# Performance work log

Measured on AMD Instinct MI355X. Metric: run time of the kernel, lower is better.

## Reference

```python
import jax, jax.numpy as jnp
import numpy as np

IN_CH = 512
HEADS = 8
DIM_HEAD = 64
HIDDEN = HEADS * DIM_HEAD


def rms_norm(x, g):
    # torch F.normalize(x, dim=1): x / max(||x||_2 along channel, eps)
    norm = jnp.sqrt(jnp.sum(x * x, axis=1, keepdims=True))
    xn = x / jnp.maximum(norm, 1e-12)
    return xn * g * (x.shape[1] ** 0.5)


def setup_inputs() -> dict:
    key = jax.random.key(0)
    ks = jax.random.split(key, 6)
    x = jax.random.normal(ks[0], (8, IN_CH, 8192), dtype=jnp.float32)
    g1 = jnp.ones((1, IN_CH, 1), dtype=jnp.float32)
    # Conv1d k=1 weights stored as [out, in]
    w_qkv = jax.random.normal(ks[1], (3 * HIDDEN, IN_CH), dtype=jnp.float32) * (IN_CH ** -0.5)
    w_out = jax.random.normal(ks[2], (IN_CH, HIDDEN), dtype=jnp.float32) * (HIDDEN ** -0.5)
    b_out = jax.random.normal(ks[3], (IN_CH,), dtype=jnp.float32) * 0.01
    g2 = jnp.ones((1, IN_CH, 1), dtype=jnp.float32)
    return {"x": x, "g1": g1, "w_qkv": w_qkv, "w_out": w_out, "b_out": b_out, "g2": g2}


def reference(x, g1, w_qkv, w_out, b_out, g2):
    b, c, l = x.shape
    h, dh = HEADS, DIM_HEAD
    scale = dh ** -0.5
    xn = rms_norm(x, g1)
    # 1x1 conv == channel matmul: [b,3*hidden,l]
    qkv = jnp.einsum('oc,bcl->bol', w_qkv, xn)
    q, k, v = jnp.split(qkv, 3, axis=1)
    q = q.reshape(b, h, dh, l)
    k = k.reshape(b, h, dh, l)
    v = v.reshape(b, h, dh, l)
    q = jax.nn.softmax(q, axis=2) * scale  # softmax over head-dim channels
    k = jax.nn.softmax(k, axis=3)          # softmax over sequence
    context = jnp.einsum('bhdn,bhen->bhde', k, v)  # [b,h,dh,dh]
    out = jnp.einsum('bhde,bhdn->bhen', context, q)
    out = out.reshape(b, h * dh, l)
    out = jnp.einsum('oc,bcl->bol', w_out, out) + b_out[None, :, None]
    return rms_norm(out, g2)
```

## Files before the change

kernel.cpp:

```cpp
#include <hip/hip_runtime.h>
#include <hip/hip_bf16.h>


typedef short short8 __attribute__((ext_vector_type(8)));
typedef short short4v __attribute__((ext_vector_type(4)));
typedef float f32x4 __attribute__((ext_vector_type(4)));
typedef unsigned short ushort;

#define SQRT512 22.627416997969522f

__device__ __forceinline__ ushort f2bf(float f){
  union{float f; unsigned u;} v; v.f = f;
  unsigned r = v.u + 0x7fffu + ((v.u >> 16) & 1u);
  return (ushort)(r >> 16);
}

__device__ __forceinline__ void gload16(const void* g, void* l){
  __builtin_amdgcn_global_load_lds(
      (const __attribute__((address_space(1))) unsigned int*)(unsigned long long)g,
      (__attribute__((address_space(3))) unsigned int*)(unsigned int)(unsigned long long)l,
      16, 0, 0);
}

__global__ void k_prep_w1(const float* __restrict__ wqkv, const float* __restrict__ g1,
                          ushort* __restrict__ W1){
  int i = blockIdx.x * 256 + threadIdx.x;
  int c = i & 511;
  W1[i] = f2bf(wqkv[i] * g1[c] * SQRT512);
}

__global__ __launch_bounds__(256) void k_xt(const float* __restrict__ x,
                                            ushort* __restrict__ Xt,
                                            float* __restrict__ invnorm){
  __shared__ __align__(16) ushort tile[64*132];
  __shared__ float ssq[4][64];
  int b = blockIdx.y, lb = blockIdx.x;
  int t = threadIdx.x, lane = t & 63, crow = t >> 6;
  const float* xb = x + ((size_t)b*512)*8192 + (size_t)lb*64;
  float acc = 0.f;
  for(int c0 = 0; c0 < 512; c0 += 128){
    __syncthreads();
    for(int cc = crow; cc < 128; cc += 4){
      float v = xb[(size_t)(c0+cc)*8192 + lane];
      acc += v*v;
      tile[lane*132 + cc] = f2bf(v);
    }
    __syncthreads();
    ushort* dst = Xt + ((size_t)(b*8192 + lb*64))*512 + c0;
    int ch = t & 31;
    for(int r = t >> 5; r < 64; r += 8){
      short4v vv = *(const short4v*)&tile[r*132 + ch*4];
      *(short4v*)(dst + (size_t)r*512 + ch*4) = vv;
    }
  }
  ssq[crow][lane] = acc;
  __syncthreads();
  if(t < 64){
    float s = ssq[0][t] + ssq[1][t] + ssq[2][t] + ssq[3][t];
    invnorm[b*8192 + lb*64 + t] = 1.f / fmaxf(sqrtf(s), 1e-12f);
  }
}

__global__ __launch_bounds__(512,1) void k_qkv(
    const ushort* __restrict__ W1, const ushort* __restrict__ Xt,
    const float* __restrict__ invnorm,
    ushort* __restrict__ Qt, float* __restrict__ ctxp, float* __restrict__ kpart){
  __shared__ __align__(16) union U {
    ushort buf[2][24576];
    struct { ushort P[16384]; ushort Vb[16384]; } e;
  } S;
  __shared__ float ksum[128];

  int bid = blockIdx.x;
  int wg  = (bid & 7)*384 + (bid >> 3);
  int b   = wg / 384;
  int rem = wg % 384;
  bool isQ = rem < 128;
  int t = threadIdx.x, lane = t & 63, w = t >> 6;
  int rsub = lane >> 3;
  int pc   = (lane & 7) ^ rsub;

  int r = 0, ct2 = 0, hb = 0, ct = 0;
  const ushort* Abase = W1;
  const ushort* Bbase;
  if(isQ){ r = rem >> 5; ct2 = rem & 31;
    Abase = W1 + (size_t)(r*128)*512;
    Bbase = Xt + ((size_t)(b*8192 + ct2*256))*512;
  } else { int kv = rem - 128; hb = kv >> 6; ct = kv & 63;
    Bbase = Xt + ((size_t)(b*8192 + ct*128))*512;
  }
  if(t < 128) ksum[t] = 0.f;

  f32x4 acc[4][4] = {};

  auto stage = [&](int ks, int cb){
    int goff = ks*64 + pc*8;
    ushort* A  = S.buf[cb];
    ushort* Bl = S.buf[cb] + (isQ ? 8192 : 16384);
    if(isQ){
#pragma unroll
      for(int j = 0; j < 2; ++j){ int m = w*2 + j;
        gload16(Abase + (size_t)(m*8 + rsub)*512 + goff, A + m*512); }
#pragma unroll
      for(int j = 0; j < 4; ++j){ int m = w*4 + j;
        gload16(Bbase + (size_t)(m*8 + rsub)*512 + goff, Bl + m*512); }
    } else {
#pragma unroll
      for(int j = 0; j < 4; ++j){ int m = w*4 + j;
        int row = (m < 16) ? (512 + hb*128 + m*8 + rsub)
                           : (1024 + hb*128 + (m-16)*8 + rsub);
        gload16(W1 + (size_t)row*512 + goff, A + m*512); }
#pragma unroll
      for(int j = 0; j < 2; ++j){ int m = w*2 + j;
        gload16(Bbase + (size_t)(m*8 + rsub)*512 + goff, Bl + m*512); }
    }
  };

  auto compute = [&](int cb){
    ushort* A  = S.buf[cb];
    ushort* Bl = S.buf[cb] + (isQ ? 8192 : 16384);
    int aw = isQ ? (w >> 2) : (w >> 1);
    int bw = isQ ? (w & 3)  : (w & 1);
#pragma unroll
    for(int kk = 0; kk < 2; ++kk){
      int g = kk*4 + (lane >> 4);
      short8 af[4], bf[4];
#pragma unroll
      for(int m4 = 0; m4 < 4; ++m4){ int ra = aw*64 + m4*16 + (lane & 15);
        af[m4] = *(const short8*)&A[ra*64 + (g ^ (ra & 7))*8]; }
#pragma unroll
      for(int n4 = 0; n4 < 4; ++n4){ int rb = bw*64 + n4*16 + (lane & 15);
        bf[n4] = *(const short8*)&Bl[rb*64 + (g ^ (rb & 7))*8]; }
#pragma unroll
      for(int m4 = 0; m4 < 4; ++m4)
#pragma unroll
        for(int n4 = 0; n4 < 4; ++n4)
          acc[m4][n4] = __builtin_amdgcn_mfma_f32_16x16x32_bf16(af[m4], bf[n4], acc[m4][n4], 0,0,0);
    }
  };

  stage(0, 0);
  int cur = 0;
#pragma unroll
  for(int ks = 0; ks < 8; ++ks){
    if(ks < 7) stage(ks + 1, cur ^ 1);
    if(ks < 7) asm volatile("s_waitcnt vmcnt(6)" ::: "memory");
    else       asm volatile("s_waitcnt vmcnt(0)" ::: "memory");
    __builtin_amdgcn_s_barrier();
    compute(cur);
    asm volatile("s_waitcnt lgkmcnt(0)" ::: "memory");
    __builtin_amdgcn_s_barrier();
    cur ^= 1;
  }

  if(isQ){
    int wr = w >> 2, wc = w & 3;
    float cs[4];
    const float* invb = invnorm + b*8192 + ct2*256;
#pragma unroll
    for(int n4 = 0; n4 < 4; ++n4) cs[n4] = invb[wc*64 + n4*16 + (lane & 15)];
    float mx[4] = {-3e38f,-3e38f,-3e38f,-3e38f};
#pragma unroll
    for(int m4 = 0; m4 < 4; ++m4)
#pragma unroll
      for(int n4 = 0; n4 < 4; ++n4)
#pragma unroll
        for(int j = 0; j < 4; ++j){
          float v = acc[m4][n4][j]*cs[n4];
          acc[m4][n4][j] = v;
          mx[n4] = fmaxf(mx[n4], v);
        }
#pragma unroll
    for(int n4 = 0; n4 < 4; ++n4){
      mx[n4] = fmaxf(mx[n4], __shfl_xor(mx[n4], 16));
      mx[n4] = fmaxf(mx[n4], __shfl_xor(mx[n4], 32));
    }
    float sm[4] = {0.f,0.f,0.f,0.f};
#pragma unroll
    for(int m4 = 0; m4 < 4; ++m4)
#pragma unroll
      for(int n4 = 0; n4 < 4; ++n4)
#pragma unroll
        for(int j = 0; j < 4; ++j){
          float e = __expf(acc[m4][n4][j] - mx[n4]);
          acc[m4][n4][j] = e;
          sm[n4] += e;
        }
    float inv[4];
#pragma unroll
    for(int n4 = 0; n4 < 4; ++n4){
      sm[n4] += __shfl_xor(sm[n4], 16);
      sm[n4] += __shfl_xor(sm[n4], 32);
      inv[n4] = 0.125f / sm[n4];
    }
#pragma unroll
    for(int n4 = 0; n4 < 4; ++n4){
      int col = ct2*256 + wc*64 + n4*16 + (lane & 15);
      ushort* dst = Qt + ((size_t)(b*8192 + col))*512 + r*128 + wr*64 + (lane >> 4)*4;
#pragma unroll
      for(int m4 = 0; m4 < 4; ++m4){
        short4v p;
#pragma unroll
        for(int j = 0; j < 4; ++j) p[j] = (short)f2bf(acc[m4][n4][j]*inv[n4]);
        *(short4v*)(dst + m4*16) = p;
      }
    }
  } else {
    int wr2 = w >> 1, bw = w & 1;
    bool isK = (w < 4);
    float cs[4];
    const float* invb = invnorm + b*8192 + ct*128;
#pragma unroll
    for(int n4 = 0; n4 < 4; ++n4) cs[n4] = invb[bw*64 + n4*16 + (lane & 15)];
#pragma unroll
    for(int m4 = 0; m4 < 4; ++m4)
#pragma unroll
      for(int j = 0; j < 4; ++j){
        int row = wr2*64 + m4*16 + (lane >> 4)*4 + j;
        float rs = 0.f;
#pragma unroll
        for(int n4 = 0; n4 < 4; ++n4){
          int lcol = bw*64 + n4*16 + (lane & 15);
          float val = acc[m4][n4][j]*cs[n4];
          if(isK){
            float e = __expf(val); rs += e;
            S.e.P[row*128 + ((lcol >> 3) ^ (row & 7))*8 + (lcol & 7)] = f2bf(e);
          } else {
            int er = row - 128;
            S.e.Vb[er*128 + ((lcol >> 3) ^ (er & 7))*8 + (lcol & 7)] = f2bf(val);
          }
        }
        if(isK) atomicAdd(&ksum[row], rs);
      }
    __syncthreads();
    if(t < 128) kpart[(size_t)ct*4096 + b*512 + hb*128 + t] = ksum[t];
    int hq = w >> 2, rq = w & 3;
    f32x4 c2[4] = {};
#pragma unroll
    for(int kk = 0; kk < 4; ++kk){
      int g = kk*4 + (lane >> 4);
      int da = hq*64 + rq*16 + (lane & 15);
      short8 pa = *(const short8*)&S.e.P[da*128 + (g ^ (da & 7))*8];
#pragma unroll
      for(int n4 = 0; n4 < 4; ++n4){
        int eb = hq*64 + n4*16 + (lane & 15);
        short8 vb = *(const short8*)&S.e.Vb[eb*128 + (g ^ (eb & 7))*8];
        c2[n4] = __builtin_amdgcn_mfma_f32_16x16x32_bf16(pa, vb, c2[n4], 0,0,0);
      }
    }
    float* dst = ctxp + ((size_t)((b*8 + hb*2 + hq)*64 + ct))*4096;
#pragma unroll
    for(int n4 = 0; n4 < 4; ++n4)
#pragma unroll
      for(int j = 0; j < 4; ++j){
        int d64 = rq*16 + (lane >> 4)*4 + j;
        int e   = n4*16 + (lane & 15);
        dst[d64*64 + e] = c2[n4][j];
      }
  }
}

__global__ void k_invz(const float* __restrict__ kpart, float* __restrict__ invZ){
  int row = blockIdx.x*256 + threadIdx.x;
  float s = 0.f;
  for(int c = 0; c < 64; ++c) s += kpart[(size_t)c*4096 + row];
  invZ[row] = 1.f / s;
}

__global__ void k_m2(const float* __restrict__ ctxp, const float* __restrict__ invZ,
                     const float* __restrict__ Wout, ushort* __restrict__ M2){
  __shared__ __align__(16) ushort ctxl[4096];
  int bh = blockIdx.x, b = bh >> 3, h = bh & 7;
  int t = threadIdx.x, lane = t & 63, w = t >> 6;
  for(int i = t; i < 4096; i += 512){
    float s = 0.f;
    for(int sp = 0; sp < 64; ++sp) s += ctxp[((size_t)(bh*64 + sp))*4096 + i];
    int d = i >> 6, e = i & 63;
    s *= invZ[bh*64 + d];
    ctxl[(e >> 3)*512 + d*8 + (e & 7)] = f2bf(s);
  }
  __syncthreads();
  f32x4 acc[4][4] = {};
#pragma unroll
  for(int kk = 0; kk < 2; ++kk){
    int g = kk*4 + (lane >> 4);
    short8 bf[4];
#pragma unroll
    for(int n4 = 0; n4 < 4; ++n4)
      bf[n4] = *(const short8*)&ctxl[g*512 + (n4*16 + (lane & 15))*8];
    int e0 = (lane >> 4)*8 + kk*32;
#pragma unroll
    for(int m4 = 0; m4 < 4; ++m4){
      int o = w*64 + m4*16 + (lane & 15);
      const float* wp = Wout + (size_t)o*512 + h*64 + e0;
      float4 w0 = *(const float4*)(wp);
      float4 w1 = *(const float4*)(wp + 4);
      short8 af;
      af[0]=(short)f2bf(w0.x); af[1]=(short)f2bf(w0.y); af[2]=(short)f2bf(w0.z); af[3]=(short)f2bf(w0.w);
      af[4]=(short)f2bf(w1.x); af[5]=(short)f2bf(w1.y); af[6]=(short)f2bf(w1.z); af[7]=(short)f2bf(w1.w);
#pragma unroll
      for(int n4 = 0; n4 < 4; ++n4)
        acc[m4][n4] = __builtin_amdgcn_mfma_f32_16x16x32_bf16(af, bf[n4], acc[m4][n4], 0,0,0);
    }
  }
  ushort* dst = M2 + (size_t)b*512*512 + h*64;
#pragma unroll
  for(int m4 = 0; m4 < 4; ++m4)
#pragma unroll
    for(int n4 = 0; n4 < 4; ++n4)
#pragma unroll
      for(int j = 0; j < 4; ++j){
        int o = w*64 + m4*16 + (lane >> 4)*4 + j;
        int d = n4*16 + (lane & 15);
        dst[(size_t)o*512 + d] = f2bf(acc[m4][n4][j]);
      }
}

__global__ __launch_bounds__(512,2) void k_out(const ushort* __restrict__ M2,
                                               const ushort* __restrict__ Qt,
                                               const float* __restrict__ bout,
                                               const float* __restrict__ g2,
                                               float* __restrict__ out){
  __shared__ __align__(16) ushort A[16384];
  __shared__ __align__(16) ushort Bs[2048];
  __shared__ float colss[64];
  __shared__ float bo[512], gg[512];
  int bid = blockIdx.x;
  int wg = (bid & 7)*128 + (bid >> 3);
  int b = wg >> 7, lb = wg & 127;
  int t = threadIdx.x, lane = t & 63, w = t >> 6;
  bo[t & 511] = bout[t & 511];
  gg[t & 511] = g2[t & 511];
  if(t < 64) colss[t] = 0.f;
  const ushort* Abase = M2 + (size_t)b*262144;
  const ushort* Bbase = Qt + ((size_t)(b*8192 + lb*64))*512;
  int rsub = lane >> 2;
  int pc   = (lane & 3) ^ ((lane >> 3) & 3);
  f32x4 acc[4][4] = {};
  for(int ks = 0; ks < 16; ++ks){
    int goff = ks*32 + pc*8;
#pragma unroll
    for(int j = 0; j < 4; ++j){
      int m = w*4 + j;
      gload16(Abase + (size_t)(m*16 + rsub)*512 + goff, &A[m*512]);
    }
    if(w >= 4){
      int m = w - 4;
      gload16(Bbase + (size_t)(m*16 + rsub)*512 + goff, &Bs[m*512]);
    }
    __syncthreads();
    int g = lane >> 4;
    short8 bf[4];
#pragma unroll
    for(int n4 = 0; n4 < 4; ++n4){
      int rb = n4*16 + (lane & 15);
      bf[n4] = *(const short8*)&Bs[rb*32 + (g ^ ((rb >> 1) & 3))*8];
    }
#pragma unroll
    for(int m4 = 0; m4 < 4; ++m4){
      int ra = w*64 + m4*16 + (lane & 15);
      short8 af = *(const short8*)&A[ra*32 + (g ^ ((ra >> 1) & 3))*8];
#pragma unroll
      for(int n4 = 0; n4 < 4; ++n4)
        acc[m4][n4] = __builtin_amdgcn_mfma_f32_16x16x32_bf16(af, bf[n4], acc[m4][n4], 0,0,0);
    }
    __syncthreads();
  }
  float ps[4] = {0.f,0.f,0.f,0.f};
#pragma unroll
  for(int m4 = 0; m4 < 4; ++m4)
#pragma unroll
    for(int j = 0; j < 4; ++j){
      int o = w*64 + m4*16 + (lane >> 4)*4 + j;
      float bb = bo[o];
#pragma unroll
      for(int n4 = 0; n4 < 4; ++n4){
        float v = acc[m4][n4][j] + bb;
        acc[m4][n4][j] = v;
        ps[n4] += v*v;
      }
    }
#pragma unroll
  for(int n4 = 0; n4 < 4; ++n4) atomicAdd(&colss[n4*16 + (lane & 15)], ps[n4]);
  __syncthreads();
  float csc[4];
#pragma unroll
  for(int n4 = 0; n4 < 4; ++n4)
    csc[n4] = SQRT512 / fmaxf(sqrtf(colss[n4*16 + (lane & 15)]), 1e-12f);
  float* obase = out + ((size_t)b*512)*8192 + lb*64;
#pragma unroll
  for(int m4 = 0; m4 < 4; ++m4)
#pragma unroll
    for(int j = 0; j < 4; ++j){
      int o = w*64 + m4*16 + (lane >> 4)*4 + j;
      float gv = gg[o];
#pragma unroll
      for(int n4 = 0; n4 < 4; ++n4)
        obase[(size_t)o*8192 + n4*16 + (lane & 15)] = acc[m4][n4][j]*csc[n4]*gv;
    }
}

extern "C" void kernel_launch(void* const* d_in, const int* in_sizes, int n_in,
                              void* d_out, int out_size, void* d_ws, size_t ws_size,
                              hipStream_t stream){
  const float* x    = (const float*)d_in[0];
  const float* g1   = (const float*)d_in[1];
  const float* wqkv = (const float*)d_in[2];
  const float* wout = (const float*)d_in[3];
  const float* bout = (const float*)d_in[4];
  const float* g2   = (const float*)d_in[5];
  float* out = (float*)d_out;
  char* ws = (char*)d_ws;
  const size_t MB = 1024*1024;
  ushort* Qt      = (ushort*)(ws);
  float*  ctxp    = (float*) (ws + 64*MB);
  ushort* W1      = (ushort*)(ws + 132*MB);
  float*  invnorm = (float*) (ws + 134*MB);
  float*  kpart   = (float*) (ws + 135*MB);
  float*  invZ    = (float*) (ws + 136*MB);
  ushort* M2      = (ushort*)(ws + 137*MB);
  ushort* Xt = (ushort*)d_out;

  k_prep_w1<<<3072, 256, 0, stream>>>(wqkv, g1, W1);
  k_xt<<<dim3(128, 8), 256, 0, stream>>>(x, Xt, invnorm);
  k_qkv<<<3072, 512, 0, stream>>>(W1, Xt, invnorm, Qt, ctxp, kpart);
  k_invz<<<16, 256, 0, stream>>>(kpart, invZ);
  k_m2<<<64, 512, 0, stream>>>(ctxp, invZ, wout, M2);
  k_out<<<1024, 512, 0, stream>>>(M2, Qt, bout, g2, out);
}
```

Measured before the change: 402.7 us.

## Halve k_qkv LDS footprint to allow more resident blocks per CU

```diff
diff --git a/kernel.cpp b/kernel.cpp
--- a/kernel.cpp
+++ b/kernel.cpp
@@ -61,13 +61,13 @@
   }
 }
 
-__global__ __launch_bounds__(512,1) void k_qkv(
+__global__ __launch_bounds__(512,4) void k_qkv(
     const ushort* __restrict__ W1, const ushort* __restrict__ Xt,
     const float* __restrict__ invnorm,
     ushort* __restrict__ Qt, float* __restrict__ ctxp, float* __restrict__ kpart){
   __shared__ __align__(16) union U {
-    ushort buf[2][24576];
-    struct { ushort P[16384]; ushort Vb[16384]; } e;
+    ushort buf[2][12288];
+    struct { ushort P[8192]; ushort Vb[8192]; } e;
   } S;
   __shared__ float ksum[128];
 
@@ -75,18 +75,19 @@
   int wg  = (bid & 7)*384 + (bid >> 3);
   int b   = wg / 384;
   int rem = wg % 384;
-  bool isQ = rem < 128;
+  int grp = rem / 12, s = rem % 12;
+  bool isQ = (s < 4);
   int t = threadIdx.x, lane = t & 63, w = t >> 6;
-  int rsub = lane >> 3;
-  int pc   = (lane & 7) ^ rsub;
+  int rsub = lane >> 2;
+  int pc   = (lane & 3) ^ ((lane >> 3) & 3);
 
   int r = 0, ct2 = 0, hb = 0, ct = 0;
-  const ushort* Abase = W1;
+  const ushort* Aq = W1;
   const ushort* Bbase;
-  if(isQ){ r = rem >> 5; ct2 = rem & 31;
-    Abase = W1 + (size_t)(r*128)*512;
+  if(isQ){ r = s; ct2 = grp;
+    Aq = W1 + (size_t)(r*128)*512;
     Bbase = Xt + ((size_t)(b*8192 + ct2*256))*512;
-  } else { int kv = rem - 128; hb = kv >> 6; ct = kv & 63;
+  } else { int t2 = s - 4; ct = 2*grp + (t2 & 1); hb = t2 >> 1;
     Bbase = Xt + ((size_t)(b*8192 + ct*128))*512;
   }
   if(t < 128) ksum[t] = 0.f;
@@ -94,63 +95,54 @@
   f32x4 acc[4][4] = {};
 
   auto stage = [&](int ks, int cb){
-    int goff = ks*64 + pc*8;
-    ushort* A  = S.buf[cb];
-    ushort* Bl = S.buf[cb] + (isQ ? 8192 : 16384);
+    int goff = ks*32 + pc*8;
     if(isQ){
-#pragma unroll
-      for(int j = 0; j < 2; ++j){ int m = w*2 + j;
-        gload16(Abase + (size_t)(m*8 + rsub)*512 + goff, A + m*512); }
-#pragma unroll
-      for(int j = 0; j < 4; ++j){ int m = w*4 + j;
-        gload16(Bbase + (size_t)(m*8 + rsub)*512 + goff, Bl + m*512); }
+      ushort* A  = S.buf[cb];
+      ushort* Bl = S.buf[cb] + 4096;
+      gload16(Aq    + (size_t)(w*16 + rsub)*512 + goff, A + w*512);
+      gload16(Bbase + (size_t)(w*32 + rsub)*512 + goff, Bl + w*1024);
+      gload16(Bbase + (size_t)(w*32 + 16 + rsub)*512 + goff, Bl + w*1024 + 512);
     } else {
-#pragma unroll
-      for(int j = 0; j < 4; ++j){ int m = w*4 + j;
-        int row = (m < 16) ? (512 + hb*128 + m*8 + rsub)
-                           : (1024 + hb*128 + (m-16)*8 + rsub);
-        gload16(W1 + (size_t)row*512 + goff, A + m*512); }
-#pragma unroll
-      for(int j = 0; j < 2; ++j){ int m = w*2 + j;
-        gload16(Bbase + (size_t)(m*8 + rsub)*512 + goff, Bl + m*512); }
+      ushort* A  = S.buf[cb];
+      ushort* Bl = S.buf[cb] + 8192;
+      int lr0 = w*32 + rsub;
+      int gr0 = (w < 4) ? (512 + hb*128 + lr0) : (1024 + hb*128 + (lr0 - 128));
+      gload16(W1 + (size_t)gr0*512 + goff, A + w*1024);
+      gload16(W1 + (size_t)(gr0 + 16)*512 + goff, A + w*1024 + 512);
+      gload16(Bbase + (size_t)(w*16 + rsub)*512 + goff, Bl + w*512);
     }
   };
 
   auto compute = [&](int cb){
-    ushort* A  = S.buf[cb];
-    ushort* Bl = S.buf[cb] + (isQ ? 8192 : 16384);
-    int aw = isQ ? (w >> 2) : (w >> 1);
-    int bw = isQ ? (w & 3)  : (w & 1);
-#pragma unroll
-    for(int kk = 0; kk < 2; ++kk){
-      int g = kk*4 + (lane >> 4);
-      short8 af[4], bf[4];
-#pragma unroll
-      for(int m4 = 0; m4 < 4; ++m4){ int ra = aw*64 + m4*16 + (lane & 15);
-        af[m4] = *(const short8*)&A[ra*64 + (g ^ (ra & 7))*8]; }
-#pragma unroll
-      for(int n4 = 0; n4 < 4; ++n4){ int rb = bw*64 + n4*16 + (lane & 15);
-        bf[n4] = *(const short8*)&Bl[rb*64 + (g ^ (rb & 7))*8]; }
-#pragma unroll
-      for(int m4 = 0; m4 < 4; ++m4)
-#pragma unroll
-        for(int n4 = 0; n4 < 4; ++n4)
-          acc[m4][n4] = __builtin_amdgcn_mfma_f32_16x16x32_bf16(af[m4], bf[n4], acc[m4][n4], 0,0,0);
-    }
+    const ushort *A, *Bl; int aw, bw;
+    if(isQ){ A = S.buf[cb]; Bl = S.buf[cb] + 4096; aw = w >> 2; bw = w & 3; }
+    else   { A = S.buf[cb]; Bl = S.buf[cb] + 8192; aw = w >> 1; bw = w & 1; }
+    int g = lane >> 4;
+    short8 af[4], bf[4];
+#pragma unroll
+    for(int m4 = 0; m4 < 4; ++m4){ int ra = aw*64 + m4*16 + (lane & 15);
+      af[m4] = *(const short8*)&A[ra*32 + (g ^ ((ra >> 1) & 3))*8]; }
+#pragma unroll
+    for(int n4 = 0; n4 < 4; ++n4){ int rb = bw*64 + n4*16 + (lane & 15);
+      bf[n4] = *(const short8*)&Bl[rb*32 + (g ^ ((rb >> 1) & 3))*8]; }
+#pragma unroll
+    for(int m4 = 0; m4 < 4; ++m4)
+#pragma unroll
+      for(int n4 = 0; n4 < 4; ++n4)
+        acc[m4][n4] = __builtin_amdgcn_mfma_f32_16x16x32_bf16(af[m4], bf[n4], acc[m4][n4], 0,0,0);
   };
 
   stage(0, 0);
-  int cur = 0;
-#pragma unroll
-  for(int ks = 0; ks < 8; ++ks){
-    if(ks < 7) stage(ks + 1, cur ^ 1);
-    if(ks < 7) asm volatile("s_waitcnt vmcnt(6)" ::: "memory");
-    else       asm volatile("s_waitcnt vmcnt(0)" ::: "memory");
+#pragma unroll
+  for(int ks = 0; ks < 16; ++ks){
+    int cur = ks & 1;
+    if(ks < 15){ stage(ks + 1, cur ^ 1);
+                 asm volatile("s_waitcnt vmcnt(3)" ::: "memory"); }
+    else       { asm volatile("s_waitcnt vmcnt(0)" ::: "memory"); }
     __builtin_amdgcn_s_barrier();
     compute(cur);
     asm volatile("s_waitcnt lgkmcnt(0)" ::: "memory");
     __builtin_amdgcn_s_barrier();
-    cur ^= 1;
   }
 
   if(isQ){
@@ -212,42 +204,48 @@
     const float* invb = invnorm + b*8192 + ct*128;
 #pragma unroll
     for(int n4 = 0; n4 < 4; ++n4) cs[n4] = invb[bw*64 + n4*16 + (lane & 15)];
-#pragma unroll
-    for(int m4 = 0; m4 < 4; ++m4)
-#pragma unroll
-      for(int j = 0; j < 4; ++j){
-        int row = wr2*64 + m4*16 + (lane >> 4)*4 + j;
-        float rs = 0.f;
-#pragma unroll
-        for(int n4 = 0; n4 < 4; ++n4){
-          int lcol = bw*64 + n4*16 + (lane & 15);
-          float val = acc[m4][n4][j]*cs[n4];
-          if(isK){
-            float e = __expf(val); rs += e;
-            S.e.P[row*128 + ((lcol >> 3) ^ (row & 7))*8 + (lcol & 7)] = f2bf(e);
-          } else {
-            int er = row - 128;
-            S.e.Vb[er*128 + ((lcol >> 3) ^ (er & 7))*8 + (lcol & 7)] = f2bf(val);
-          }
-        }
-        if(isK) atomicAdd(&ksum[row], rs);
-      }
-    __syncthreads();
-    if(t < 128) kpart[(size_t)ct*4096 + b*512 + hb*128 + t] = ksum[t];
     int hq = w >> 2, rq = w & 3;
     f32x4 c2[4] = {};
 #pragma unroll
-    for(int kk = 0; kk < 4; ++kk){
-      int g = kk*4 + (lane >> 4);
-      int da = hq*64 + rq*16 + (lane & 15);
-      short8 pa = *(const short8*)&S.e.P[da*128 + (g ^ (da & 7))*8];
-#pragma unroll
-      for(int n4 = 0; n4 < 4; ++n4){
-        int eb = hq*64 + n4*16 + (lane & 15);
-        short8 vb = *(const short8*)&S.e.Vb[eb*128 + (g ^ (eb & 7))*8];
-        c2[n4] = __builtin_amdgcn_mfma_f32_16x16x32_bf16(pa, vb, c2[n4], 0,0,0);
-      }
-    }
+    for(int hl = 0; hl < 2; ++hl){
+      __syncthreads();
+      if(bw == hl){
+#pragma unroll
+        for(int m4 = 0; m4 < 4; ++m4)
+#pragma unroll
+          for(int j = 0; j < 4; ++j){
+            int row = wr2*64 + m4*16 + (lane >> 4)*4 + j;
+            float rs = 0.f;
+#pragma unroll
+            for(int n4 = 0; n4 < 4; ++n4){
+              int lc = n4*16 + (lane & 15);
+              float val = acc[m4][n4][j]*cs[n4];
+              if(isK){
+                float e = __expf(val); rs += e;
+                S.e.P[row*64 + ((lc >> 3) ^ (row & 7))*8 + (lc & 7)] = f2bf(e);
+              } else {
+                int er = row - 128;
+                S.e.Vb[er*64 + ((lc >> 3) ^ (er & 7))*8 + (lc & 7)] = f2bf(val);
+              }
+            }
+            if(isK) atomicAdd(&ksum[row], rs);
+          }
+      }
+      __syncthreads();
+#pragma unroll
+      for(int kk = 0; kk < 2; ++kk){
+        int g2 = kk*4 + (lane >> 4);
+        int da = hq*64 + rq*16 + (lane & 15);
+        short8 pa = *(const short8*)&S.e.P[da*64 + (g2 ^ (da & 7))*8];
+#pragma unroll
+        for(int n4 = 0; n4 < 4; ++n4){
+          int eb = hq*64 + n4*16 + (lane & 15);
+          short8 vb = *(const short8*)&S.e.Vb[eb*64 + (g2 ^ (eb & 7))*8];
+          c2[n4] = __builtin_amdgcn_mfma_f32_16x16x32_bf16(pa, vb, c2[n4], 0,0,0);
+        }
+      }
+    }
+    if(t < 128) kpart[(size_t)ct*4096 + b*512 + hb*128 + t] = ksum[t];
     float* dst = ctxp + ((size_t)((b*8 + hb*2 + hq)*64 + ct))*4096;
 #pragma unroll
     for(int n4 = 0; n4 < 4; ++n4)
```

Measured after the change: 402.9 us. About the same (+0.0%).
